# Performance work log

Measured on AMD Instinct MI355X. Metric: run time of the kernel, lower is better.

## Reference

```python
import jax, jax.numpy as jnp
import numpy as np

HEADS = 8
DIM_HEAD = 64
MAX_REL = 200  # max_rel_dist


def setup_inputs() -> dict:
    key = jax.random.key(0)
    ks = jax.random.split(key, 5)
    B, N, D = 4, 2048, 512
    x = jax.random.normal(ks[0], (B, N, D), dtype=jnp.float32)
    temporal_mask = jax.random.randint(ks[1], (N, N), 0, 2, dtype=jnp.int32)
    gamma = jnp.ones((D,), jnp.float32)
    beta = jnp.zeros((D,), jnp.float32)
    Wqkv = jax.random.normal(ks[2], (D, 3 * HEADS * DIM_HEAD), dtype=jnp.float32) * 0.02
    Wout = jax.random.normal(ks[3], (HEADS * DIM_HEAD, D), dtype=jnp.float32) * 0.02
    bout = jnp.zeros((D,), jnp.float32)
    rel_table = jax.random.normal(ks[4], (2 * MAX_REL - 1,), dtype=jnp.float32) * 0.02
    return {"x": x, "gamma": gamma, "beta": beta, "Wqkv": Wqkv, "Wout": Wout,
            "bout": bout, "rel_table": rel_table, "temporal_mask": temporal_mask}


def reference(x, gamma, beta, Wqkv, Wout, bout, rel_table, temporal_mask):
    B, N, D = x.shape
    scale = DIM_HEAD ** -0.5
    # LayerNorm
    mu = jnp.mean(x, axis=-1, keepdims=True)
    var = jnp.mean(jnp.square(x - mu), axis=-1, keepdims=True)
    xn = (x - mu) * jax.lax.rsqrt(var + 1e-5) * gamma + beta
    # QKV projection (no bias), split heads: b n (h d) -> b h n d
    qkv = xn @ Wqkv  # [B, N, 3*H*d]
    q, k, v = jnp.split(qkv, 3, axis=-1)
    split = lambda t: t.reshape(B, N, HEADS, DIM_HEAD).transpose(0, 2, 1, 3)
    q, k, v = split(q), split(k), split(v)
    # scores with learned relative-position bias
    dots = jnp.einsum('bhnd,bhmd->bhnm', q, k) * scale  # [B,H,N,N]
    idx = jnp.arange(N)
    rel = jnp.clip(idx[:, None] - idx[None, :], -(MAX_REL - 1), MAX_REL - 1) + MAX_REL - 1
    dots = dots + rel_table[rel][None, None, :, :]
    # temporal mask (0 -> -inf); large negative for grad safety
    dots = jnp.where(temporal_mask[None, None, :, :] == 0, jnp.float32(-1e9), dots)
    attn = jax.nn.softmax(dots, axis=-1)
    out = jnp.einsum('bhnm,bhmd->bhnd', attn, v)
    out = out.transpose(0, 2, 1, 3).reshape(B, N, HEADS * DIM_HEAD)
    return out @ Wout + bout
```

## Files before the change

kernel.cpp:

```cpp
#include <hip/hip_runtime.h>

typedef __attribute__((ext_vector_type(8))) short bf16x8;
typedef __attribute__((ext_vector_type(4))) short bf16x4;
typedef __attribute__((ext_vector_type(4))) float f32x4;
typedef unsigned short ushort_t;

#define B_ 4
#define H_ 8
#define N_ 2048
#define D_ 512
#define MAXREL 199

__device__ __forceinline__ ushort_t f2bf(float f) {
    union { float f; unsigned u; } v; v.f = f;
    unsigned r = v.u + 0x7fffu + ((v.u >> 16) & 1u);
    return (ushort_t)(r >> 16);
}
__device__ __forceinline__ ushort_t f2bf_fast(float f) {
    union { float f; unsigned u; } v; v.f = f;
    return (ushort_t)((v.u + 0x8000u) >> 16);
}
__device__ __forceinline__ float bf2f(ushort_t u) {
    union { unsigned u; float f; } v; v.u = ((unsigned)u) << 16;
    return v.f;
}

__global__ __launch_bounds__(256) void ln_kernel(const float* __restrict__ x,
                                                 const float* __restrict__ gamma,
                                                 const float* __restrict__ beta,
                                                 ushort_t* __restrict__ xn) {
    __shared__ float sbuf[4];
    const int row = blockIdx.x;
    const int t = threadIdx.x;
    const float* xr = x + (size_t)row * D_;

    float v0 = xr[t];
    float v1 = xr[t + 256];

    float s = v0 + v1;
    for (int o = 32; o > 0; o >>= 1) s += __shfl_down(s, o);
    if ((t & 63) == 0) sbuf[t >> 6] = s;
    __syncthreads();
    float mu = (sbuf[0] + sbuf[1] + sbuf[2] + sbuf[3]) * (1.0f / D_);
    __syncthreads();

    float d0 = v0 - mu, d1 = v1 - mu;
    float s2 = d0 * d0 + d1 * d1;
    for (int o = 32; o > 0; o >>= 1) s2 += __shfl_down(s2, o);
    if ((t & 63) == 0) sbuf[t >> 6] = s2;
    __syncthreads();
    float var = (sbuf[0] + sbuf[1] + sbuf[2] + sbuf[3]) * (1.0f / D_);
    float rs = rsqrtf(var + 1e-5f);

    ushort_t* yr = xn + (size_t)row * D_;
    yr[t]       = f2bf(d0 * rs * gamma[t]       + beta[t]);
    yr[t + 256] = f2bf(d1 * rs * gamma[t + 256] + beta[t + 256]);
}

__global__ __launch_bounds__(256) void wtrans_kernel(const float* __restrict__ W,
                                                     ushort_t* __restrict__ Wt,
                                                     int K, int Nn) {
    __shared__ float tile[32][33];
    const int bx = blockIdx.x * 32;
    const int by = blockIdx.y * 32;
    const int tx = threadIdx.x & 31, ty = threadIdx.x >> 5;
    #pragma unroll
    for (int i = 0; i < 32; i += 8)
        tile[ty + i][tx] = W[(size_t)(by + ty + i) * Nn + bx + tx];
    __syncthreads();
    #pragma unroll
    for (int i = 0; i < 32; i += 8)
        Wt[(size_t)(bx + ty + i) * K + by + tx] = f2bf(tile[tx][ty + i]);
}

__global__ __launch_bounds__(256) void bias_pack_kernel(const float* __restrict__ rel,
                                                        const int* __restrict__ mask,
                                                        ushort_t* __restrict__ bp) {
    int idx = blockIdx.x * 256 + threadIdx.x;
    int n = idx >> 11, m = idx & 2047;
    int dl = n - m;
    dl = dl < -MAXREL ? -MAXREL : (dl > MAXREL ? MAXREL : dl);
    float v = (mask[idx] == 0) ? -1e9f : rel[dl + MAXREL];
    int jt = m >> 6, m16 = m & 15, nt = (m >> 4) & 3;
    bp[((size_t)n * 32 + jt) * 64 + m16 * 4 + nt] = f2bf(v);
}

__global__ __launch_bounds__(256) void gemm_qkv(const ushort_t* __restrict__ A,
                                                const ushort_t* __restrict__ Bt,
                                                ushort_t* __restrict__ qb,
                                                ushort_t* __restrict__ kb,
                                                ushort_t* __restrict__ vb) {
    __shared__ ushort_t As[128 * 32];
    __shared__ ushort_t Bs[128 * 32];
    const int t = threadIdx.x;
    const int lane = t & 63, w = t >> 6;
    const int m16 = lane & 15, quad = lane >> 4;
    const int wr = w >> 1, wc = w & 1;
    const int r0 = blockIdx.y * 128, c0 = blockIdx.x * 128;

    f32x4 acc[4][4];
    #pragma unroll
    for (int i = 0; i < 4; i++)
        #pragma unroll
        for (int j = 0; j < 4; j++) acc[i][j] = (f32x4){0.f, 0.f, 0.f, 0.f};

    for (int k0 = 0; k0 < D_; k0 += 32) {
        #pragma unroll
        for (int i = 0; i < 2; i++) {
            int f = t + i * 256;
            int row = f >> 2, kq = f & 3;
            *(bf16x8*)(As + f * 8) = *(const bf16x8*)(A + (size_t)(r0 + row) * D_ + k0 + kq * 8);
            *(bf16x8*)(Bs + f * 8) = *(const bf16x8*)(Bt + (size_t)(c0 + row) * D_ + k0 + kq * 8);
        }
        __syncthreads();
        bf16x8 af[4], bfr[4];
        #pragma unroll
        for (int rt = 0; rt < 4; rt++)
            af[rt] = *(const bf16x8*)(As + (wr * 64 + rt * 16 + m16) * 32 + quad * 8);
        #pragma unroll
        for (int ct = 0; ct < 4; ct++)
            bfr[ct] = *(const bf16x8*)(Bs + (wc * 64 + ct * 16 + m16) * 32 + quad * 8);
        #pragma unroll
        for (int rt = 0; rt < 4; rt++)
            #pragma unroll
            for (int ct = 0; ct < 4; ct++)
                acc[rt][ct] = __builtin_amdgcn_mfma_f32_16x16x32_bf16(af[rt], bfr[ct], acc[rt][ct], 0, 0, 0);
        __syncthreads();
    }

    #pragma unroll
    for (int ct = 0; ct < 4; ct++) {
        int cc = c0 + wc * 64 + ct * 16;
        int which = cc >> 9;
        int h = (cc >> 6) & 7;
        int d = (cc & 63) + m16;
        #pragma unroll
        for (int rt = 0; rt < 4; rt++) {
            int rowb = r0 + wr * 64 + rt * 16 + quad * 4;
            int b = rowb >> 11, n0 = rowb & 2047;
            if (which == 0) {
                #pragma unroll
                for (int r = 0; r < 4; r++)
                    qb[((size_t)((b * H_ + h) * N_ + n0 + r)) * 64 + d] = f2bf(acc[rt][ct][r] * 0.125f);
            } else if (which == 1) {
                #pragma unroll
                for (int r = 0; r < 4; r++)
                    kb[((size_t)((b * H_ + h) * N_ + n0 + r)) * 64 + d] = f2bf(acc[rt][ct][r]);
            } else {
                union { ushort_t u4[4]; unsigned long long ll; } pk;
                #pragma unroll
                for (int r = 0; r < 4; r++) pk.u4[r] = f2bf(acc[rt][ct][r]);
                *(unsigned long long*)(vb + ((size_t)((b * H_ + h) * 64 + d)) * N_ + n0) = pk.ll;
            }
        }
    }
}

__global__ __launch_bounds__(256) void gemm_out(const ushort_t* __restrict__ A,
                                                const ushort_t* __restrict__ Bt,
                                                const float* __restrict__ bias,
                                                float* __restrict__ C) {
    __shared__ ushort_t As[128 * 32];
    __shared__ ushort_t Bs[128 * 32];
    const int t = threadIdx.x;
    const int lane = t & 63, w = t >> 6;
    const int m16 = lane & 15, quad = lane >> 4;
    const int wr = w >> 1, wc = w & 1;
    const int r0 = blockIdx.y * 128, c0 = blockIdx.x * 128;

    f32x4 acc[4][4];
    #pragma unroll
    for (int i = 0; i < 4; i++)
        #pragma unroll
        for (int j = 0; j < 4; j++) acc[i][j] = (f32x4){0.f, 0.f, 0.f, 0.f};

    for (int k0 = 0; k0 < D_; k0 += 32) {
        #pragma unroll
        for (int i = 0; i < 2; i++) {
            int f = t + i * 256;
            int row = f >> 2, kq = f & 3;
            *(bf16x8*)(As + f * 8) = *(const bf16x8*)(A + (size_t)(r0 + row) * D_ + k0 + kq * 8);
            *(bf16x8*)(Bs + f * 8) = *(const bf16x8*)(Bt + (size_t)(c0 + row) * D_ + k0 + kq * 8);
        }
        __syncthreads();
        bf16x8 af[4], bfr[4];
        #pragma unroll
        for (int rt = 0; rt < 4; rt++)
            af[rt] = *(const bf16x8*)(As + (wr * 64 + rt * 16 + m16) * 32 + quad * 8);
        #pragma unroll
        for (int ct = 0; ct < 4; ct++)
            bfr[ct] = *(const bf16x8*)(Bs + (wc * 64 + ct * 16 + m16) * 32 + quad * 8);
        #pragma unroll
        for (int rt = 0; rt < 4; rt++)
            #pragma unroll
            for (int ct = 0; ct < 4; ct++)
                acc[rt][ct] = __builtin_amdgcn_mfma_f32_16x16x32_bf16(af[rt], bfr[ct], acc[rt][ct], 0, 0, 0);
        __syncthreads();
    }

    #pragma unroll
    for (int rt = 0; rt < 4; rt++) {
        #pragma unroll
        for (int ct = 0; ct < 4; ct++) {
            int col = c0 + wc * 64 + ct * 16 + m16;
            int row0 = r0 + wr * 64 + rt * 16 + quad * 4;
            float bv = bias[col];
            #pragma unroll
            for (int r = 0; r < 4; r++)
                C[(size_t)(row0 + r) * 512 + col] = acc[rt][ct][r] + bv;
        }
    }
}

__global__ __launch_bounds__(256, 2) void attn_mfma(const ushort_t* __restrict__ qb,
                                                    const ushort_t* __restrict__ kb,
                                                    const ushort_t* __restrict__ vb,
                                                    const ushort_t* __restrict__ bp,
                                                    ushort_t* __restrict__ attn) {
    __shared__ ushort_t Ks[2][64 * 64];
    __shared__ ushort_t Vs[2][64 * 64];
    __shared__ ushort_t p_s[4][2][16][72];

    const int t = threadIdx.x;
    const int w = t >> 6, lane = t & 63;
    const int m16 = lane & 15, quad = lane >> 4;
    const int id = blockIdx.x;
    const int bh = id & 31;
    const int qt = id >> 5;
    const int b = bh >> 3, h = bh & 7;
    const int n0w = qt * 128 + w * 32;

    const int srow0 = t >> 3, scb = t & 7;
    const int srow1 = srow0 + 32;
    const int soff0 = srow0 * 64 + (scb ^ (srow0 & 7)) * 8;
    const int soff1 = srow1 * 64 + (scb ^ (srow1 & 7)) * 8;
    const ushort_t* kgbase = kb + ((size_t)bh * N_) * 64;
    const ushort_t* vgbase = vb + ((size_t)bh * 64) * N_;

    const ushort_t* qpb = qb + ((size_t)(bh * N_ + n0w + m16)) * 64 + quad * 8;
    bf16x8 qa[2][2];
    qa[0][0] = *(const bf16x8*)(qpb);
    qa[0][1] = *(const bf16x8*)(qpb + 32);
    qa[1][0] = *(const bf16x8*)(qpb + 16 * 64);
    qa[1][1] = *(const bf16x8*)(qpb + 16 * 64 + 32);

    {
        bf16x8 k0 = *(const bf16x8*)(kgbase + (size_t)srow0 * 64 + scb * 8);
        bf16x8 k1 = *(const bf16x8*)(kgbase + (size_t)srow1 * 64 + scb * 8);
        bf16x8 v0 = *(const bf16x8*)(vgbase + (size_t)srow0 * N_ + scb * 8);
        bf16x8 v1 = *(const bf16x8*)(vgbase + (size_t)srow1 * N_ + scb * 8);
        *(bf16x8*)(&Ks[0][soff0]) = k0;
        *(bf16x8*)(&Ks[0][soff1]) = k1;
        *(bf16x8*)(&Vs[0][soff0]) = v0;
        *(bf16x8*)(&Vs[0][soff1]) = v1;
    }
    __syncthreads();

    f32x4 o[2][4];
    #pragma unroll
    for (int mf = 0; mf < 2; mf++)
        #pragma unroll
        for (int nt = 0; nt < 4; nt++) o[mf][nt] = (f32x4){0.f, 0.f, 0.f, 0.f};
    float rsum[2][4] = {};

    for (int jt = 0; jt < 32; jt++) {
        const int buf = jt & 1;
        const int j0 = jt * 64;
        const bool more = (jt < 31);

        bf16x8 kst0, kst1, vst0, vst1;
        if (more) {
            const ushort_t* kg = kgbase + (size_t)(j0 + 64) * 64;
            const ushort_t* vg = vgbase + (j0 + 64);
            kst0 = *(const bf16x8*)(kg + (size_t)srow0 * 64 + scb * 8);
            kst1 = *(const bf16x8*)(kg + (size_t)srow1 * 64 + scb * 8);
            vst0 = *(const bf16x8*)(vg + (size_t)srow0 * N_ + scb * 8);
            vst1 = *(const bf16x8*)(vg + (size_t)srow1 * N_ + scb * 8);
        }

        bf16x4 bcur[2][4];
        #pragma unroll
        for (int mf = 0; mf < 2; mf++)
            #pragma unroll
            for (int r = 0; r < 4; r++) {
                int n = n0w + mf * 16 + quad * 4 + r;
                bcur[mf][r] = *(const bf16x4*)(bp + ((size_t)n * 32 + jt) * 64 + m16 * 4);
            }

        f32x4 s[2][4];
        #pragma unroll
        for (int nt = 0; nt < 4; nt++) {
            int kr = nt * 16 + m16;
            bf16x8 kf0 = *(const bf16x8*)(&Ks[buf][kr * 64 + ((quad) ^ (kr & 7)) * 8]);
            bf16x8 kf1 = *(const bf16x8*)(&Ks[buf][kr * 64 + ((quad + 4) ^ (kr & 7)) * 8]);
            #pragma unroll
            for (int mf = 0; mf < 2; mf++) {
                f32x4 a2 = (f32x4){0.f, 0.f, 0.f, 0.f};
                a2 = __builtin_amdgcn_mfma_f32_16x16x32_bf16(qa[mf][0], kf0, a2, 0, 0, 0);
                a2 = __builtin_amdgcn_mfma_f32_16x16x32_bf16(qa[mf][1], kf1, a2, 0, 0, 0);
                s[mf][nt] = a2;
            }
        }

        #pragma unroll
        for (int mf = 0; mf < 2; mf++)
            #pragma unroll
            for (int nt = 0; nt < 4; nt++)
                #pragma unroll
                for (int r = 0; r < 4; r++) {
                    float p = __expf(s[mf][nt][r] + bf2f((ushort_t)bcur[mf][r][nt]));
                    rsum[mf][r] += p;
                    p_s[w][mf][quad * 4 + r][nt * 16 + m16] = f2bf_fast(p);
                }

        bf16x8 pa[2][2];
        #pragma unroll
        for (int mf = 0; mf < 2; mf++) {
            pa[mf][0] = *(const bf16x8*)(&p_s[w][mf][m16][quad * 8]);
            pa[mf][1] = *(const bf16x8*)(&p_s[w][mf][m16][32 + quad * 8]);
        }

        #pragma unroll
        for (int nt = 0; nt < 4; nt++) {
            int d = nt * 16 + m16;
            bf16x8 vf0 = *(const bf16x8*)(&Vs[buf][d * 64 + ((quad) ^ (d & 7)) * 8]);
            bf16x8 vf1 = *(const bf16x8*)(&Vs[buf][d * 64 + ((quad + 4) ^ (d & 7)) * 8]);
            #pragma unroll
            for (int mf = 0; mf < 2; mf++) {
                o[mf][nt] = __builtin_amdgcn_mfma_f32_16x16x32_bf16(pa[mf][0], vf0, o[mf][nt], 0, 0, 0);
                o[mf][nt] = __builtin_amdgcn_mfma_f32_16x16x32_bf16(pa[mf][1], vf1, o[mf][nt], 0, 0, 0);
            }
        }

        if (more) {
            *(bf16x8*)(&Ks[buf ^ 1][soff0]) = kst0;
            *(bf16x8*)(&Ks[buf ^ 1][soff1]) = kst1;
            *(bf16x8*)(&Vs[buf ^ 1][soff0]) = vst0;
            *(bf16x8*)(&Vs[buf ^ 1][soff1]) = vst1;
        }
        __syncthreads();
    }

    #pragma unroll
    for (int mf = 0; mf < 2; mf++)
        #pragma unroll
        for (int r = 0; r < 4; r++) {
            float t2 = rsum[mf][r];
            t2 += __shfl_xor(t2, 1);
            t2 += __shfl_xor(t2, 2);
            t2 += __shfl_xor(t2, 4);
            t2 += __shfl_xor(t2, 8);
            float inv = 1.0f / t2;
            int n = n0w + mf * 16 + quad * 4 + r;
            ushort_t* orow = attn + ((size_t)(b * N_ + n)) * 512 + h * 64 + m16;
            #pragma unroll
            for (int nt = 0; nt < 4; nt++) orow[nt * 16] = f2bf(o[mf][nt][r] * inv);
        }
}

extern "C" void kernel_launch(void* const* d_in, const int* in_sizes, int n_in,
                              void* d_out, int out_size, void* d_ws, size_t ws_size,
                              hipStream_t stream) {
    const float* x     = (const float*)d_in[0];
    const float* gamma = (const float*)d_in[1];
    const float* beta  = (const float*)d_in[2];
    const float* Wqkv  = (const float*)d_in[3];
    const float* Wout  = (const float*)d_in[4];
    const float* bout  = (const float*)d_in[5];
    const float* rel   = (const float*)d_in[6];
    const int*   mask  = (const int*)d_in[7];
    float* out = (float*)d_out;

    char* wsb = (char*)d_ws;
    ushort_t* xn    = (ushort_t*)(wsb);
    ushort_t* attnb = (ushort_t*)(wsb + ( 8u << 20));
    ushort_t* qb    = (ushort_t*)(wsb + (16u << 20));
    ushort_t* kb    = (ushort_t*)(wsb + (24u << 20));
    ushort_t* vb    = (ushort_t*)(wsb + (32u << 20));
    ushort_t* WqkvT = (ushort_t*)(wsb + (40u << 20));
    ushort_t* WoutT = (ushort_t*)(wsb + (42u << 20));
    ushort_t* bp    = (ushort_t*)(wsb + (44u << 20));

    wtrans_kernel<<<dim3(1536 / 32, 512 / 32), 256, 0, stream>>>(Wqkv, WqkvT, 512, 1536);
    wtrans_kernel<<<dim3(512 / 32, 512 / 32), 256, 0, stream>>>(Wout, WoutT, 512, 512);
    bias_pack_kernel<<<(N_ * N_) / 256, 256, 0, stream>>>(rel, mask, bp);

    ln_kernel<<<B_ * N_, 256, 0, stream>>>(x, gamma, beta, xn);

    gemm_qkv<<<dim3(1536 / 128, 8192 / 128), 256, 0, stream>>>(xn, WqkvT, qb, kb, vb);

    attn_mfma<<<512, 256, 0, stream>>>(qb, kb, vb, bp, attnb);

    gemm_out<<<dim3(512 / 128, 8192 / 128), 256, 0, stream>>>(attnb, WoutT, bout, out);
}
```

Baseline: 224.7 us.

## Use direct global-to-LDS loads in GEMMs, smaller out tiles, swizzled P buffer

Replaces the register-staged global-to-shared copies in both GEMMs with global_load_lds direct transfers, which removes VGPR round trips. The output GEMM tile shrinks from 128 to 64 rows, doubling its grid to fill more CUs. The attention kernel's P staging buffer moves from padded rows to an XOR-swizzled layout to avoid bank conflicts with less LDS, and its launch bounds ask for 3 blocks per CU. These changes risk register spills under the tighter occupancy target and lower arithmetic intensity in the smaller GEMM tile.

```diff
diff --git a/kernel.cpp b/kernel.cpp
--- a/kernel.cpp
+++ b/kernel.cpp
@@ -23,6 +23,12 @@
 __device__ __forceinline__ float bf2f(ushort_t u) {
     union { unsigned u; float f; } v; v.u = ((unsigned)u) << 16;
     return v.f;
+}
+__device__ __forceinline__ void gl_lds16(const ushort_t* g, ushort_t* l) {
+    __builtin_amdgcn_global_load_lds(
+        (const __attribute__((address_space(1))) void*)g,
+        (__attribute__((address_space(3))) void*)l,
+        16, 0, 0);
 }
 
 __global__ __launch_bounds__(256) void ln_kernel(const float* __restrict__ x,
@@ -98,6 +104,11 @@
     const int wr = w >> 1, wc = w & 1;
     const int r0 = blockIdx.y * 128, c0 = blockIdx.x * 128;
 
+    const ushort_t* Ag = A  + (size_t)(r0 + (t >> 2)) * D_ + (t & 3) * 8;
+    const ushort_t* Bg = Bt + (size_t)(c0 + (t >> 2)) * D_ + (t & 3) * 8;
+    ushort_t* AsW = As + w * 512;
+    ushort_t* BsW = Bs + w * 512;
+
     f32x4 acc[4][4];
     #pragma unroll
     for (int i = 0; i < 4; i++)
@@ -105,13 +116,10 @@
         for (int j = 0; j < 4; j++) acc[i][j] = (f32x4){0.f, 0.f, 0.f, 0.f};
 
     for (int k0 = 0; k0 < D_; k0 += 32) {
-        #pragma unroll
-        for (int i = 0; i < 2; i++) {
-            int f = t + i * 256;
-            int row = f >> 2, kq = f & 3;
-            *(bf16x8*)(As + f * 8) = *(const bf16x8*)(A + (size_t)(r0 + row) * D_ + k0 + kq * 8);
-            *(bf16x8*)(Bs + f * 8) = *(const bf16x8*)(Bt + (size_t)(c0 + row) * D_ + k0 + kq * 8);
-        }
+        gl_lds16(Ag + k0, AsW);
+        gl_lds16(Ag + k0 + (size_t)64 * D_, AsW + 2048);
+        gl_lds16(Bg + k0, BsW);
+        gl_lds16(Bg + k0 + (size_t)64 * D_, BsW + 2048);
         __syncthreads();
         bf16x8 af[4], bfr[4];
         #pragma unroll
@@ -160,66 +168,67 @@
                                                 const ushort_t* __restrict__ Bt,
                                                 const float* __restrict__ bias,
                                                 float* __restrict__ C) {
-    __shared__ ushort_t As[128 * 32];
+    __shared__ ushort_t As[64 * 32];
     __shared__ ushort_t Bs[128 * 32];
     const int t = threadIdx.x;
     const int lane = t & 63, w = t >> 6;
     const int m16 = lane & 15, quad = lane >> 4;
     const int wr = w >> 1, wc = w & 1;
-    const int r0 = blockIdx.y * 128, c0 = blockIdx.x * 128;
-
-    f32x4 acc[4][4];
-    #pragma unroll
-    for (int i = 0; i < 4; i++)
+    const int r0 = blockIdx.y * 64, c0 = blockIdx.x * 128;
+
+    const ushort_t* Ag = A  + (size_t)(r0 + (t >> 2)) * D_ + (t & 3) * 8;
+    const ushort_t* Bg = Bt + (size_t)(c0 + (t >> 2)) * D_ + (t & 3) * 8;
+    ushort_t* AsW = As + w * 512;
+    ushort_t* BsW = Bs + w * 512;
+
+    f32x4 acc[2][4];
+    #pragma unroll
+    for (int i = 0; i < 2; i++)
         #pragma unroll
         for (int j = 0; j < 4; j++) acc[i][j] = (f32x4){0.f, 0.f, 0.f, 0.f};
 
     for (int k0 = 0; k0 < D_; k0 += 32) {
-        #pragma unroll
-        for (int i = 0; i < 2; i++) {
-            int f = t + i * 256;
-            int row = f >> 2, kq = f & 3;
-            *(bf16x8*)(As + f * 8) = *(const bf16x8*)(A + (size_t)(r0 + row) * D_ + k0 + kq * 8);
-            *(bf16x8*)(Bs + f * 8) = *(const bf16x8*)(Bt + (size_t)(c0 + row) * D_ + k0 + kq * 8);
-        }
+        gl_lds16(Ag + k0, AsW);
+        gl_lds16(Bg + k0, BsW);
+        gl_lds16(Bg + k0 + (size_t)64 * D_, BsW + 2048);
         __syncthreads();
-        bf16x8 af[4], bfr[4];
-        #pragma unroll
-        for (int rt = 0; rt < 4; rt++)
-            af[rt] = *(const bf16x8*)(As + (wr * 64 + rt * 16 + m16) * 32 + quad * 8);
-        #pragma unroll
-        for (int ct = 0; ct < 4; ct++)
-            bfr[ct] = *(const bf16x8*)(Bs + (wc * 64 + ct * 16 + m16) * 32 + quad * 8);
-        #pragma unroll
-        for (int rt = 0; rt < 4; rt++)
-            #pragma unroll
-            for (int ct = 0; ct < 4; ct++)
-                acc[rt][ct] = __builtin_amdgcn_mfma_f32_16x16x32_bf16(af[rt], bfr[ct], acc[rt][ct], 0, 0, 0);
+        bf16x8 af[2], bfr[4];
+        #pragma unroll
+        for (int mf = 0; mf < 2; mf++)
+            af[mf] = *(const bf16x8*)(As + (wr * 32 + mf * 16 + m16) * 32 + quad * 8);
+        #pragma unroll
+        for (int nt = 0; nt < 4; nt++)
+            bfr[nt] = *(const bf16x8*)(Bs + (wc * 64 + nt * 16 + m16) * 32 + quad * 8);
+        #pragma unroll
+        for (int mf = 0; mf < 2; mf++)
+            #pragma unroll
+            for (int nt = 0; nt < 4; nt++)
+                acc[mf][nt] = __builtin_amdgcn_mfma_f32_16x16x32_bf16(af[mf], bfr[nt], acc[mf][nt], 0, 0, 0);
         __syncthreads();
     }
 
     #pragma unroll
-    for (int rt = 0; rt < 4; rt++) {
-        #pragma unroll
-        for (int ct = 0; ct < 4; ct++) {
-            int col = c0 + wc * 64 + ct * 16 + m16;
-            int row0 = r0 + wr * 64 + rt * 16 + quad * 4;
+    for (int mf = 0; mf < 2; mf++) {
+        #pragma unroll
+        for (int nt = 0; nt < 4; nt++) {
+            int col = c0 + wc * 64 + nt * 16 + m16;
+            int row0 = r0 + wr * 32 + mf * 16 + quad * 4;
             float bv = bias[col];
             #pragma unroll
             for (int r = 0; r < 4; r++)
-                C[(size_t)(row0 + r) * 512 + col] = acc[rt][ct][r] + bv;
-        }
-    }
-}
-
-__global__ __launch_bounds__(256, 2) void attn_mfma(const ushort_t* __restrict__ qb,
+                C[(size_t)(row0 + r) * 512 + col] = acc[mf][nt][r] + bv;
+        }
+    }
+}
+
+__global__ __launch_bounds__(256, 3) void attn_mfma(const ushort_t* __restrict__ qb,
                                                     const ushort_t* __restrict__ kb,
                                                     const ushort_t* __restrict__ vb,
                                                     const ushort_t* __restrict__ bp,
                                                     ushort_t* __restrict__ attn) {
     __shared__ ushort_t Ks[2][64 * 64];
     __shared__ ushort_t Vs[2][64 * 64];
-    __shared__ ushort_t p_s[4][2][16][72];
+    __shared__ ushort_t p_s[4 * 2][16 * 64];
 
     const int t = threadIdx.x;
     const int w = t >> 6, lane = t & 63;
@@ -303,21 +312,27 @@
         }
 
         #pragma unroll
-        for (int mf = 0; mf < 2; mf++)
-            #pragma unroll
-            for (int nt = 0; nt < 4; nt++)
+        for (int mf = 0; mf < 2; mf++) {
+            ushort_t* pw = p_s[w * 2 + mf];
+            #pragma unroll
+            for (int nt = 0; nt < 4; nt++) {
+                int chunk = nt * 2 + (m16 >> 3), pos = m16 & 7;
                 #pragma unroll
                 for (int r = 0; r < 4; r++) {
                     float p = __expf(s[mf][nt][r] + bf2f((ushort_t)bcur[mf][r][nt]));
                     rsum[mf][r] += p;
-                    p_s[w][mf][quad * 4 + r][nt * 16 + m16] = f2bf_fast(p);
+                    int row = quad * 4 + r;
+                    pw[row * 64 + ((chunk ^ (row & 7)) << 3) + pos] = f2bf_fast(p);
                 }
+            }
+        }
 
         bf16x8 pa[2][2];
         #pragma unroll
         for (int mf = 0; mf < 2; mf++) {
-            pa[mf][0] = *(const bf16x8*)(&p_s[w][mf][m16][quad * 8]);
-            pa[mf][1] = *(const bf16x8*)(&p_s[w][mf][m16][32 + quad * 8]);
+            const ushort_t* pw = p_s[w * 2 + mf];
+            pa[mf][0] = *(const bf16x8*)(pw + m16 * 64 + ((quad ^ (m16 & 7)) << 3));
+            pa[mf][1] = *(const bf16x8*)(pw + m16 * 64 + (((quad + 4) ^ (m16 & 7)) << 3));
         }
 
         #pragma unroll
@@ -391,5 +406,5 @@
 
     attn_mfma<<<512, 256, 0, stream>>>(qb, kb, vb, bp, attnb);
 
-    gemm_out<<<dim3(512 / 128, 8192 / 128), 256, 0, stream>>>(attnb, WoutT, bout, out);
-}
+    gemm_out<<<dim3(512 / 128, 8192 / 64), 256, 0, stream>>>(attnb, WoutT, bout, out);
+}
```

Result: faster. 214.1 us (-4.7%).
